# Kernel tuning notes

Measured on AMD Instinct MI355X. Metric: run time of the kernel, lower is better.

The kernel has to match this reference:

```python
import jax, jax.numpy as jnp
import numpy as np
from jax import lax

WINDOW_SIZE = 11
SIGMA = 1.5
DATA_RANGE = 1.0
LEVELS = 4
EPS = 1e-8
DN = ('NCHW', 'OIHW', 'NCHW')


def _gauss1d(k, sigma):
    coords = jnp.arange(k, dtype=jnp.float32) - k // 2
    g = jnp.exp(-coords ** 2 / (2.0 * sigma ** 2))
    return g / g.sum()


def _blur(x, g):
    # separable depthwise Gaussian blur, VALID padding (use_padding=False)
    C = x.shape[1]
    k = g.shape[0]
    kw = jnp.broadcast_to(g.reshape(1, 1, 1, k), (C, 1, 1, k)).astype(x.dtype)
    kh = jnp.broadcast_to(g.reshape(1, 1, k, 1), (C, 1, k, 1)).astype(x.dtype)
    x = lax.conv_general_dilated(x, kw, (1, 1), 'VALID', dimension_numbers=DN, feature_group_count=C)
    x = lax.conv_general_dilated(x, kh, (1, 1), 'VALID', dimension_numbers=DN, feature_group_count=C)
    return x


def _avg_pool2(x):
    B, C, H, W = x.shape  # H, W even here (512 -> 64)
    return x.reshape(B, C, H // 2, 2, W // 2, 2).mean(axis=(3, 5))


def _ssim_level(X, Y, g):
    C1 = (0.01 * DATA_RANGE) ** 2
    C2 = (0.03 * DATA_RANGE) ** 2
    mu1 = _blur(X, g)
    mu2 = _blur(Y, g)
    sigma1_sq = _blur(X * X, g) - mu1 * mu1
    sigma2_sq = _blur(Y * Y, g) - mu2 * mu2
    sigma12 = _blur(X * Y, g) - mu1 * mu2
    cs_map = jax.nn.relu((2.0 * sigma12 + C2) / (sigma1_sq + sigma2_sq + C2))
    ssim_map = (2.0 * mu1 * mu2 + C1) / (mu1 * mu1 + mu2 * mu2 + C1) * cs_map
    return ssim_map.mean(axis=(1, 2, 3)), cs_map.mean(axis=(1, 2, 3))


def setup_inputs() -> dict:
    key = jax.random.key(0)
    kx, ky = jax.random.split(key)
    X = jax.random.uniform(kx, (16, 3, 512, 512), dtype=jnp.float32)
    Y = jax.random.uniform(ky, (16, 3, 512, 512), dtype=jnp.float32)
    return {'X': X, 'Y': Y}


def reference(X, Y):
    g = _gauss1d(WINDOW_SIZE, SIGMA)
    w = jnp.array([0.0448, 0.2856, 0.3001, 0.2363], dtype=jnp.float32)
    w = w / w.sum()
    vals = []
    for i in range(LEVELS):
        ss, cs = _ssim_level(X, Y, g)
        if i < LEVELS - 1:
            vals.append(cs)
            X = _avg_pool2(X)
            Y = _avg_pool2(Y)
        else:
            vals.append(ss)
    vals = jnp.maximum(jnp.stack(vals, axis=0), EPS)  # [levels, B]
    ms = jnp.prod(vals ** w[:, None], axis=0)
    return 1.0 - ms
```

## Files before the change

### kernel.cpp

```cpp
#include <hip/hip_runtime.h>
#include <math.h>

#define HALO 10
#define TS 32
#define INR 42
#define STR 46
#define P2_TOTAL 16320

typedef float f2 __attribute__((ext_vector_type(2)));

struct GaussW { float g[11]; };

__global__ void pool_all_kernel(
    const float* __restrict__ X0, const float* __restrict__ Y0,
    float* __restrict__ X1, float* __restrict__ Y1,
    float* __restrict__ X2, float* __restrict__ Y2,
    float* __restrict__ X3, float* __restrict__ Y3)
{
    const int gid = blockIdx.x * 256 + threadIdx.x;
    const int bc  = gid >> 12;
    const int rem = gid & 4095;
    const int R = rem >> 6, C = rem & 63;

    const float* xin = X0 + (size_t)bc * 512 * 512;
    const float* yin = Y0 + (size_t)bc * 512 * 512;
    float* x1 = X1 + (size_t)bc * 256 * 256;
    float* y1 = Y1 + (size_t)bc * 256 * 256;
    float* x2 = X2 + (size_t)bc * 128 * 128;
    float* y2 = Y2 + (size_t)bc * 128 * 128;
    float* x3 = X3 + (size_t)bc * 64 * 64;
    float* y3 = Y3 + (size_t)bc * 64 * 64;

    float tx2a = 0.f, tx2b = 0.f, ty2a = 0.f, ty2b = 0.f, tx3 = 0.f, ty3 = 0.f;
    #pragma unroll
    for (int q = 0; q < 4; ++q) {
        const float* rx = xin + (size_t)(8 * R + 2 * q) * 512 + 8 * C;
        const float* ry = yin + (size_t)(8 * R + 2 * q) * 512 + 8 * C;
        float4 a0 = *(const float4*)rx,        b0 = *(const float4*)(rx + 4);
        float4 a1 = *(const float4*)(rx + 512), b1 = *(const float4*)(rx + 516);
        float4 c0v = *(const float4*)ry,        d0 = *(const float4*)(ry + 4);
        float4 c1v = *(const float4*)(ry + 512), d1 = *(const float4*)(ry + 516);
        float4 p1x, p1y;
        p1x.x = 0.25f * (a0.x + a0.y + a1.x + a1.y);
        p1x.y = 0.25f * (a0.z + a0.w + a1.z + a1.w);
        p1x.z = 0.25f * (b0.x + b0.y + b1.x + b1.y);
        p1x.w = 0.25f * (b0.z + b0.w + b1.z + b1.w);
        p1y.x = 0.25f * (c0v.x + c0v.y + c1v.x + c1v.y);
        p1y.y = 0.25f * (c0v.z + c0v.w + c1v.z + c1v.w);
        p1y.z = 0.25f * (d0.x + d0.y + d1.x + d1.y);
        p1y.w = 0.25f * (d0.z + d0.w + d1.z + d1.w);
        *(float4*)(x1 + (size_t)(4 * R + q) * 256 + 4 * C) = p1x;
        *(float4*)(y1 + (size_t)(4 * R + q) * 256 + 4 * C) = p1y;
        if ((q & 1) == 0) {
            tx2a = p1x.x + p1x.y; tx2b = p1x.z + p1x.w;
            ty2a = p1y.x + p1y.y; ty2b = p1y.z + p1y.w;
        } else {
            float2 p2x = { 0.25f * (tx2a + p1x.x + p1x.y), 0.25f * (tx2b + p1x.z + p1x.w) };
            float2 p2y = { 0.25f * (ty2a + p1y.x + p1y.y), 0.25f * (ty2b + p1y.z + p1y.w) };
            *(float2*)(x2 + (size_t)(2 * R + (q >> 1)) * 128 + 2 * C) = p2x;
            *(float2*)(y2 + (size_t)(2 * R + (q >> 1)) * 128 + 2 * C) = p2y;
            if (q == 1) { tx3 = p2x.x + p2x.y; ty3 = p2y.x + p2y.y; }
            else {
                x3[(size_t)R * 64 + C] = 0.25f * (tx3 + p2x.x + p2x.y);
                y3[(size_t)R * 64 + C] = 0.25f * (ty3 + p2y.x + p2y.y);
            }
        }
    }
}

__global__ __launch_bounds__(256, 5) void ssim_all_kernel(
    const float* __restrict__ X0, const float* __restrict__ Y0,
    const float* __restrict__ X1, const float* __restrict__ Y1,
    const float* __restrict__ X2, const float* __restrict__ Y2,
    const float* __restrict__ X3, const float* __restrict__ Y3,
    GaussW gw, float* __restrict__ P2)
{
    __shared__ float U[4 * TS * STR];
    __shared__ float red[2];

    const int tid = threadIdx.x;
    const int t   = blockIdx.x;

    int l, rem;
    if      (t < 12288) { l = 0; rem = t; }
    else if (t < 15360) { l = 1; rem = t - 12288; }
    else if (t < 16128) { l = 2; rem = t - 15360; }
    else                { l = 3; rem = t - 16128; }
    const int l2   = 4 - l;
    const int H    = 512 >> l;
    const int W    = H;
    const int Hout = H - HALO;
    const int bc   = rem >> (2 * l2);
    const int r2   = rem & ((1 << (2 * l2)) - 1);
    const int by   = r2 >> l2, bx = r2 & ((1 << l2) - 1);
    const int r0   = by * TS, c0 = bx * TS;
    const float* X = (l == 0) ? X0 : (l == 1) ? X1 : (l == 2) ? X2 : X3;
    const float* Y = (l == 0) ? Y0 : (l == 1) ? Y1 : (l == 2) ? Y2 : Y3;
    const size_t base = (size_t)bc * H * W;

    for (int idx = tid; idx < INR * 22; idx += 256) {
        int rr = idx / 22, pp = idx - rr * 22;
        int gr = r0 + rr, gc = c0 + 2 * pp;
        float2 xv = make_float2(0.f, 0.f), yv = make_float2(0.f, 0.f);
        if (gr < H && gc < W) {
            xv = *(const float2*)(X + base + (size_t)gr * W + gc);
            yv = *(const float2*)(Y + base + (size_t)gr * W + gc);
        }
        *(float2*)&U[rr * STR + 2 * pp]              = xv;
        *(float2*)&U[INR * STR + rr * STR + 2 * pp]  = yv;
    }
    __syncthreads();

    const int rr  = tid >> 2;
    const int seg = tid & 3;
    const int ccb = seg * 8;
    float x[20], y[20];
    if (tid < 168) {
        #pragma unroll
        for (int u = 0; u < 10; ++u) {
            *(f2*)&x[2 * u] = *(const f2*)&U[rr * STR + ccb + 2 * u];
            *(f2*)&y[2 * u] = *(const f2*)&U[INR * STR + rr * STR + ccb + 2 * u];
        }
    }
    __syncthreads();

    if (tid < 168) {
        #pragma unroll
        for (int p = 0; p < 4; ++p) {
            f2 ax = {0.f, 0.f}, ay = {0.f, 0.f};
            #pragma unroll
            for (int k = 0; k < 11; ++k) {
                f2 vx = { x[2 * p + k], x[2 * p + k + 1] };
                f2 vy = { y[2 * p + k], y[2 * p + k + 1] };
                ax += vx * gw.g[k];
                ay += vy * gw.g[k];
            }
            U[0 * TS * STR + (ccb + 2 * p) * STR + rr]     = ax.x;
            U[0 * TS * STR + (ccb + 2 * p + 1) * STR + rr] = ax.y;
            U[1 * TS * STR + (ccb + 2 * p) * STR + rr]     = ay.x;
            U[1 * TS * STR + (ccb + 2 * p + 1) * STR + rr] = ay.y;
        }
        #pragma unroll
        for (int i = 0; i < 9; ++i) {
            f2 xv = *(f2*)&x[2 * i];
            f2 yv = *(f2*)&y[2 * i];
            f2 a = xv + yv;
            f2 d = xv - yv;
            *(f2*)&x[2 * i] = a * a;
            *(f2*)&y[2 * i] = d * d;
        }
        #pragma unroll
        for (int p = 0; p < 4; ++p) {
            f2 as = {0.f, 0.f}, ad = {0.f, 0.f};
            #pragma unroll
            for (int k = 0; k < 11; ++k) {
                f2 vs = { x[2 * p + k], x[2 * p + k + 1] };
                f2 vd = { y[2 * p + k], y[2 * p + k + 1] };
                as += vs * gw.g[k];
                ad += vd * gw.g[k];
            }
            U[2 * TS * STR + (ccb + 2 * p) * STR + rr]     = as.x;
            U[2 * TS * STR + (ccb + 2 * p + 1) * STR + rr] = as.y;
            U[3 * TS * STR + (ccb + 2 * p) * STR + rr]     = ad.x;
            U[3 * TS * STR + (ccb + 2 * p + 1) * STR + rr] = ad.y;
        }
    }
    __syncthreads();

    float acc_s = 0.f;
    if (tid < 128) {
        const int tx = tid & 31;
        const int tg = tid >> 5;
        const int rb = tg * 8;

        f2 m1[4], m2[4], S[4], D[4];
        #define VPASS(Q, OUT)                                                    \
        {                                                                        \
            float win[18];                                                       \
            _Pragma("unroll")                                                    \
            for (int i = 0; i < 9; ++i)                                          \
                *(f2*)&win[2 * i] = *(const f2*)&U[(Q) * TS * STR + tx * STR + rb + 2 * i]; \
            _Pragma("unroll")                                                    \
            for (int h = 0; h < 4; ++h) {                                        \
                f2 a = {0.f, 0.f};                                               \
                _Pragma("unroll")                                                \
                for (int k = 0; k < 11; ++k) {                                   \
                    f2 v = { win[2 * h + k], win[2 * h + k + 1] };               \
                    a += v * gw.g[k];                                            \
                }                                                                \
                OUT[h] = a;                                                      \
            }                                                                    \
        }
        VPASS(0, m1) VPASS(1, m2) VPASS(2, S) VPASS(3, D)
        #undef VPASS

        const float C1 = 1e-4f, C2 = 9e-4f;
        #pragma unroll
        for (int o = 0; o < 8; ++o) {
            float u1 = m1[o >> 1][o & 1], u2 = m2[o >> 1][o & 1];
            float Sv = S[o >> 1][o & 1],  Dv = D[o >> 1][o & 1];
            float u1s = u1 * u1, u2s = u2 * u2, u12 = u1 * u2;
            float ssum = 0.5f  * (Sv + Dv);
            float sxy  = 0.25f * (Sv - Dv);
            float vsum = ssum - u1s - u2s;
            float v12  = sxy - u12;
            float A2   = fmaxf(2.f * v12 + C2, 0.f);
            float B1   = u1s + u2s + C1;
            float B2   = vsum + C2;
            float inv  = __builtin_amdgcn_rcpf(B1 * B2);
            float val;
            if (l != 3) {
                val = A2 * B1 * inv;
            } else {
                float A1 = 2.f * u12 + C1;
                val = A1 * A2 * inv;
            }
            bool valid = (r0 + rb + o < Hout) && (c0 + tx < Hout);
            acc_s += valid ? val : 0.f;
        }
    }

    #pragma unroll
    for (int off = 32; off; off >>= 1) acc_s += __shfl_down(acc_s, off);
    if (tid == 0)  red[0] = acc_s;
    if (tid == 64) red[1] = acc_s;
    __syncthreads();
    if (tid == 0) P2[t] = red[0] + red[1];
}

__global__ void finalize_kernel(const float* __restrict__ P2, float* __restrict__ out) {
    __shared__ float red[64][4];
    const int tid  = threadIdx.x;
    const int pair = tid >> 2;
    const int chnk = tid & 3;
    const int l = pair >> 4, b = pair & 15;
    const int off[4]  = {0, 12288, 15360, 16128};
    const int nper[4] = {768, 192, 48, 12};
    const int n4 = nper[l] >> 2;
    const float* p = P2 + off[l] + b * nper[l] + chnk * n4;
    float s = 0.f;
    for (int j = 0; j < n4; ++j) s += p[j];
    red[pair][chnk] = s;
    __syncthreads();
    if (tid < 16) {
        const int bb = tid;
        const float wraw[4] = {0.0448f, 0.2856f, 0.3001f, 0.2363f};
        float wsum = wraw[0] + wraw[1] + wraw[2] + wraw[3];
        float ms = 1.f;
        for (int ll = 0; ll < 4; ++ll) {
            int Hh = 512 >> ll;
            int Ho = Hh - HALO;
            float cnt = 3.f * (float)Ho * (float)Ho;
            float val = (red[ll * 16 + bb][0] + red[ll * 16 + bb][1] +
                         red[ll * 16 + bb][2] + red[ll * 16 + bb][3]) / cnt;
            val = fmaxf(val, 1e-8f);
            ms *= powf(val, wraw[ll] / wsum);
        }
        out[bb] = 1.f - ms;
    }
}

extern "C" void kernel_launch(void* const* d_in, const int* in_sizes, int n_in,
                              void* d_out, int out_size, void* d_ws, size_t ws_size,
                              hipStream_t stream)
{
    const float* X0 = (const float*)d_in[0];
    const float* Y0 = (const float*)d_in[1];
    float* out = (float*)d_out;
    float* ws  = (float*)d_ws;

    float* P2 = ws;
    float* X1 = ws + P2_TOTAL;
    float* Y1 = X1 + (size_t)16 * 3 * 256 * 256;
    float* X2 = Y1 + (size_t)16 * 3 * 256 * 256;
    float* Y2 = X2 + (size_t)16 * 3 * 128 * 128;
    float* X3 = Y2 + (size_t)16 * 3 * 128 * 128;
    float* Y3 = X3 + (size_t)16 * 3 * 64 * 64;

    GaussW gw;
    {
        float s = 0.f;
        for (int i = 0; i < 11; ++i) {
            float d = (float)(i - 5);
            gw.g[i] = expf(-d * d / (2.f * 1.5f * 1.5f));
            s += gw.g[i];
        }
        for (int i = 0; i < 11; ++i) gw.g[i] /= s;
    }

    hipLaunchKernelGGL(pool_all_kernel, dim3(768), dim3(256), 0, stream,
                       X0, Y0, X1, Y1, X2, Y2, X3, Y3);
    hipLaunchKernelGGL(ssim_all_kernel, dim3(16320), dim3(256), 0, stream,
                       X0, Y0, X1, Y1, X2, Y2, X3, Y3, gw, P2);
    hipLaunchKernelGGL(finalize_kernel, dim3(1), dim3(256), 0, stream, P2, out);
}
```

Before: 219.7 us.

## Fuse 2x2 pyramid pooling into level-0 SSIM tiles, split launch by level

Removes the separate pooling kernel and computes the level-1/2/3 downsampled images inside the level-0 SSIM blocks from the tile already staged in shared memory, using wave shuffles for the coarser levels. The SSIM kernel is then launched twice, first for level 0 and then for levels 1-3, so the later levels read pooled data written by the first launch. This avoids re-reading the full-resolution inputs from global memory for pooling. It adds scattered scalar global stores and shuffle work to the level-0 blocks, and raises the occupancy hint from 5 to 6 blocks, which may increase register pressure.

```diff
diff --git a/kernel.cpp b/kernel.cpp
--- a/kernel.cpp
+++ b/kernel.cpp
@@ -11,75 +11,18 @@
 
 struct GaussW { float g[11]; };
 
-__global__ void pool_all_kernel(
+__global__ __launch_bounds__(256, 6) void ssim_kernel(
     const float* __restrict__ X0, const float* __restrict__ Y0,
     float* __restrict__ X1, float* __restrict__ Y1,
     float* __restrict__ X2, float* __restrict__ Y2,
-    float* __restrict__ X3, float* __restrict__ Y3)
-{
-    const int gid = blockIdx.x * 256 + threadIdx.x;
-    const int bc  = gid >> 12;
-    const int rem = gid & 4095;
-    const int R = rem >> 6, C = rem & 63;
-
-    const float* xin = X0 + (size_t)bc * 512 * 512;
-    const float* yin = Y0 + (size_t)bc * 512 * 512;
-    float* x1 = X1 + (size_t)bc * 256 * 256;
-    float* y1 = Y1 + (size_t)bc * 256 * 256;
-    float* x2 = X2 + (size_t)bc * 128 * 128;
-    float* y2 = Y2 + (size_t)bc * 128 * 128;
-    float* x3 = X3 + (size_t)bc * 64 * 64;
-    float* y3 = Y3 + (size_t)bc * 64 * 64;
-
-    float tx2a = 0.f, tx2b = 0.f, ty2a = 0.f, ty2b = 0.f, tx3 = 0.f, ty3 = 0.f;
-    #pragma unroll
-    for (int q = 0; q < 4; ++q) {
-        const float* rx = xin + (size_t)(8 * R + 2 * q) * 512 + 8 * C;
-        const float* ry = yin + (size_t)(8 * R + 2 * q) * 512 + 8 * C;
-        float4 a0 = *(const float4*)rx,        b0 = *(const float4*)(rx + 4);
-        float4 a1 = *(const float4*)(rx + 512), b1 = *(const float4*)(rx + 516);
-        float4 c0v = *(const float4*)ry,        d0 = *(const float4*)(ry + 4);
-        float4 c1v = *(const float4*)(ry + 512), d1 = *(const float4*)(ry + 516);
-        float4 p1x, p1y;
-        p1x.x = 0.25f * (a0.x + a0.y + a1.x + a1.y);
-        p1x.y = 0.25f * (a0.z + a0.w + a1.z + a1.w);
-        p1x.z = 0.25f * (b0.x + b0.y + b1.x + b1.y);
-        p1x.w = 0.25f * (b0.z + b0.w + b1.z + b1.w);
-        p1y.x = 0.25f * (c0v.x + c0v.y + c1v.x + c1v.y);
-        p1y.y = 0.25f * (c0v.z + c0v.w + c1v.z + c1v.w);
-        p1y.z = 0.25f * (d0.x + d0.y + d1.x + d1.y);
-        p1y.w = 0.25f * (d0.z + d0.w + d1.z + d1.w);
-        *(float4*)(x1 + (size_t)(4 * R + q) * 256 + 4 * C) = p1x;
-        *(float4*)(y1 + (size_t)(4 * R + q) * 256 + 4 * C) = p1y;
-        if ((q & 1) == 0) {
-            tx2a = p1x.x + p1x.y; tx2b = p1x.z + p1x.w;
-            ty2a = p1y.x + p1y.y; ty2b = p1y.z + p1y.w;
-        } else {
-            float2 p2x = { 0.25f * (tx2a + p1x.x + p1x.y), 0.25f * (tx2b + p1x.z + p1x.w) };
-            float2 p2y = { 0.25f * (ty2a + p1y.x + p1y.y), 0.25f * (ty2b + p1y.z + p1y.w) };
-            *(float2*)(x2 + (size_t)(2 * R + (q >> 1)) * 128 + 2 * C) = p2x;
-            *(float2*)(y2 + (size_t)(2 * R + (q >> 1)) * 128 + 2 * C) = p2y;
-            if (q == 1) { tx3 = p2x.x + p2x.y; ty3 = p2y.x + p2y.y; }
-            else {
-                x3[(size_t)R * 64 + C] = 0.25f * (tx3 + p2x.x + p2x.y);
-                y3[(size_t)R * 64 + C] = 0.25f * (ty3 + p2y.x + p2y.y);
-            }
-        }
-    }
-}
-
-__global__ __launch_bounds__(256, 5) void ssim_all_kernel(
-    const float* __restrict__ X0, const float* __restrict__ Y0,
-    const float* __restrict__ X1, const float* __restrict__ Y1,
-    const float* __restrict__ X2, const float* __restrict__ Y2,
-    const float* __restrict__ X3, const float* __restrict__ Y3,
-    GaussW gw, float* __restrict__ P2)
+    float* __restrict__ X3, float* __restrict__ Y3,
+    GaussW gw, float* __restrict__ P2, int tbase)
 {
     __shared__ float U[4 * TS * STR];
     __shared__ float red[2];
 
     const int tid = threadIdx.x;
-    const int t   = blockIdx.x;
+    const int t   = blockIdx.x + tbase;
 
     int l, rem;
     if      (t < 12288) { l = 0; rem = t; }
@@ -122,6 +65,16 @@
             *(f2*)&y[2 * u] = *(const f2*)&U[INR * STR + rr * STR + ccb + 2 * u];
         }
     }
+    float p1x = 0.f, p1y = 0.f;
+    if (l == 0) {
+        const int pr = tid >> 4, pc = tid & 15;
+        f2 xa = *(const f2*)&U[(2 * pr) * STR + 2 * pc];
+        f2 xb = *(const f2*)&U[(2 * pr + 1) * STR + 2 * pc];
+        f2 ya = *(const f2*)&U[INR * STR + (2 * pr) * STR + 2 * pc];
+        f2 yb = *(const f2*)&U[INR * STR + (2 * pr + 1) * STR + 2 * pc];
+        p1x = 0.25f * (xa.x + xa.y + xb.x + xb.y);
+        p1y = 0.25f * (ya.x + ya.y + yb.x + yb.y);
+    }
     __syncthreads();
 
     if (tid < 168) {
@@ -163,6 +116,28 @@
             U[2 * TS * STR + (ccb + 2 * p + 1) * STR + rr] = as.y;
             U[3 * TS * STR + (ccb + 2 * p) * STR + rr]     = ad.x;
             U[3 * TS * STR + (ccb + 2 * p + 1) * STR + rr] = ad.y;
+        }
+    }
+
+    if (l == 0) {
+        const int pr = tid >> 4, pc = tid & 15;
+        size_t o1 = (size_t)bc * 256 * 256 + (size_t)(r0 / 2 + pr) * 256 + (c0 / 2 + pc);
+        X1[o1] = p1x;
+        Y1[o1] = p1y;
+        float sx = p1x + __shfl_xor(p1x, 1);  sx += __shfl_xor(sx, 16);
+        float sy = p1y + __shfl_xor(p1y, 1);  sy += __shfl_xor(sy, 16);
+        float p2x = 0.25f * sx, p2y = 0.25f * sy;
+        if ((tid & 17) == 0) {
+            size_t o2 = (size_t)bc * 128 * 128 + (size_t)(r0 / 4 + (pr >> 1)) * 128 + (c0 / 4 + (pc >> 1));
+            X2[o2] = p2x;
+            Y2[o2] = p2y;
+        }
+        float tx3 = p2x + __shfl_xor(p2x, 2);  tx3 += __shfl_xor(tx3, 32);
+        float ty3 = p2y + __shfl_xor(p2y, 2);  ty3 += __shfl_xor(ty3, 32);
+        if ((tid & 51) == 0) {
+            size_t o3 = (size_t)bc * 64 * 64 + (size_t)(r0 / 8 + (pr >> 2)) * 64 + (c0 / 8 + (pc >> 2));
+            X3[o3] = 0.25f * tx3;
+            Y3[o3] = 0.25f * ty3;
         }
     }
     __syncthreads();
@@ -288,9 +263,9 @@
         for (int i = 0; i < 11; ++i) gw.g[i] /= s;
     }
 
-    hipLaunchKernelGGL(pool_all_kernel, dim3(768), dim3(256), 0, stream,
-                       X0, Y0, X1, Y1, X2, Y2, X3, Y3);
-    hipLaunchKernelGGL(ssim_all_kernel, dim3(16320), dim3(256), 0, stream,
-                       X0, Y0, X1, Y1, X2, Y2, X3, Y3, gw, P2);
+    hipLaunchKernelGGL(ssim_kernel, dim3(12288), dim3(256), 0, stream,
+                       X0, Y0, X1, Y1, X2, Y2, X3, Y3, gw, P2, 0);
+    hipLaunchKernelGGL(ssim_kernel, dim3(4032), dim3(256), 0, stream,
+                       X0, Y0, X1, Y1, X2, Y2, X3, Y3, gw, P2, 12288);
     hipLaunchKernelGGL(finalize_kernel, dim3(1), dim3(256), 0, stream, P2, out);
 }
```

New measurement: 211.4 us. 3.8% less time.
